# Kernel tuning notes

Hardware: AMD Instinct MI355X
Metric: run time of the kernel (lower is better)

The kernel has to match this reference:

```python
import jax, jax.numpy as jnp
import numpy as np

B = 16; V = 30522; D = 512; H = 8; DH = 64; FF = 2048
NC = 4; NF = 30; NN = 34; FL = 64; HL = 32; NLAYERS = 2

def _pos_encoding(L, d):
    pos = np.arange(L)[:, None].astype(np.float32)
    i = np.arange(0, d, 2)[None, :].astype(np.float32)
    ang = pos / np.power(10000.0, i / d)
    pe = np.zeros((L, d), dtype=np.float32)
    pe[:, 0::2] = np.sin(ang)
    pe[:, 1::2] = np.cos(ang)
    return jnp.asarray(pe)

def _ln(x, g, b):
    m = x.mean(-1, keepdims=True)
    v = ((x - m) ** 2).mean(-1, keepdims=True)
    return (x - m) / jnp.sqrt(v + 1e-5) * g + b

def _encoder(ids, emb, Wqkv, bqkv, Wo, bo, ln1_g, ln1_b, Wff1, bff1, Wff2, bff2, ln2_g, ln2_b):
    Bx, L = ids.shape
    x = emb[ids] * jnp.sqrt(jnp.float32(D)) + _pos_encoding(L, D)
    for l in range(NLAYERS):  # torch post-norm encoder layer, relu FFN
        qkv = x @ Wqkv[l] + bqkv[l]
        q, k, v = jnp.split(qkv, 3, axis=-1)
        q = q.reshape(Bx, L, H, DH); k = k.reshape(Bx, L, H, DH); v = v.reshape(Bx, L, H, DH)
        att = jax.nn.softmax(jnp.einsum('blhd,bmhd->bhlm', q, k) / jnp.sqrt(jnp.float32(DH)), axis=-1)
        o = jnp.einsum('bhlm,bmhd->blhd', att, v).reshape(Bx, L, D) @ Wo[l] + bo[l]
        x = _ln(x + o, ln1_g[l], ln1_b[l])
        f = jax.nn.relu(x @ Wff1[l] + bff1[l]) @ Wff2[l] + bff2[l]
        x = _ln(x + f, ln2_g[l], ln2_b[l])
    return x

def _masked_mean(emb, mask):
    m = mask[..., None]
    return (emb * m).sum(1) / jnp.clip(m.sum(1), 1e-9, None)

def _solve_edges(W, adj, iters=100, lr=0.05, c=10.0):
    # differentiable proxy for the CvxpyLayer SDP relaxation: projected gradient
    # ascent on symmetric E in [0,1], maximizing sum(W*E) with quadratic penalties
    # for sum(adj*E) <= 6 and trace(E[:4,:4]) == 1 (PSD constraint dropped).
    diag4 = jnp.zeros((NN, NN)).at[jnp.arange(NC), jnp.arange(NC)].set(1.0)
    E0 = jnp.full(W.shape, 0.5)
    def step(E, _):
        s = jnp.sum(adj * E, axis=(1, 2), keepdims=True)
        d = jnp.sum(E * diag4, axis=(1, 2), keepdims=True)
        g = W - 2.0 * c * jax.nn.relu(s - 6.0) * adj - 2.0 * c * (d - 1.0) * diag4
        En = E + lr * g
        En = jnp.clip(0.5 * (En + jnp.swapaxes(En, 1, 2)), 0.0, 1.0)
        return En, None
    E, _ = jax.lax.scan(step, E0, None, length=iters)
    return E

def setup_inputs():
    key = jax.random.key(0)
    ks = jax.random.split(key, 24)
    w = lambda k, shape: (jax.random.normal(k, shape) * 0.02).astype(jnp.float32)
    return {
        'hypothesis_input_ids': jax.random.randint(ks[0], (B, NC, HL), 0, V),
        'hypothesis_attention_mask': jnp.ones((B, NC, HL), jnp.float32),
        'fact_attention_mask': jnp.ones((B, NF, FL), jnp.float32),
        'fact_input_ids': jax.random.randint(ks[1], (B, NF, FL), 0, V),
        'grounding_grounding_overlap': jax.random.uniform(ks[2], (B, NN, NN)),
        'abstract_abstract_overlap': jax.random.uniform(ks[3], (B, NN, NN)),
        'abstract_abstract_similarity': jax.random.uniform(ks[4], (B, NN, NN)),
        'question_grounding_overlap': jax.random.uniform(ks[5], (B, NN, NN)),
        'question_abstract_overlap': jax.random.uniform(ks[6], (B, NN, NN)),
        'question_abstract_similarity': jax.random.uniform(ks[7], (B, NN, NN)),
        'grounding_abstract_overlap': jax.random.uniform(ks[8], (B, NN, NN)),
        'question_question_score': w(ks[9], (B, NN, NN)),
        'labels': jax.random.randint(ks[10], (B,), 0, NC),
        'gold_similarity_scores': jax.random.normal(ks[11], (B, NC, NF)),
        'emb_table': w(ks[12], (V, D)),
        'Wqkv': w(ks[13], (NLAYERS, D, 3 * D)), 'bqkv': jnp.zeros((NLAYERS, 3 * D)),
        'Wo': w(ks[14], (NLAYERS, D, D)), 'bo': jnp.zeros((NLAYERS, D)),
        'ln1_g': jnp.ones((NLAYERS, D)), 'ln1_b': jnp.zeros((NLAYERS, D)),
        'Wff1': w(ks[15], (NLAYERS, D, FF)), 'bff1': jnp.zeros((NLAYERS, FF)),
        'Wff2': w(ks[16], (NLAYERS, FF, D)), 'bff2': jnp.zeros((NLAYERS, D)),
        'ln2_g': jnp.ones((NLAYERS, D)), 'ln2_b': jnp.zeros((NLAYERS, D)),
        'score_W': w(ks[17], (4 * D,)), 'score_b': jnp.zeros(()),
        'abs_score_W': w(ks[18], (4 * D,)), 'abs_score_b': jnp.zeros(()),
        'p_aa_overlap': jnp.ones(()), 'p_aa_sim': jnp.ones(()),
        'p_qa_overlap': jnp.ones(()), 'p_qa_sim': jnp.ones(()),
    }

def reference(hypothesis_input_ids, hypothesis_attention_mask, fact_attention_mask, fact_input_ids,
              grounding_grounding_overlap, abstract_abstract_overlap, abstract_abstract_similarity,
              question_grounding_overlap, question_abstract_overlap, question_abstract_similarity,
              grounding_abstract_overlap, question_question_score, labels, gold_similarity_scores,
              emb_table, Wqkv, bqkv, Wo, bo, ln1_g, ln1_b, Wff1, bff1, Wff2, bff2, ln2_g, ln2_b,
              score_W, score_b, abs_score_W, abs_score_b, p_aa_overlap, p_aa_sim, p_qa_overlap, p_qa_sim):
    enc = lambda ids: _encoder(ids, emb_table, Wqkv, bqkv, Wo, bo, ln1_g, ln1_b,
                               Wff1, bff1, Wff2, bff2, ln2_g, ln2_b)
    fseq = _masked_mean(enc(fact_input_ids.reshape(-1, FL)),
                        fact_attention_mask.reshape(-1, FL)).reshape(-1, NF, D)
    hseq = _masked_mean(enc(hypothesis_input_ids.reshape(-1, HL)),
                        hypothesis_attention_mask.reshape(-1, HL)).reshape(-1, NC, D)
    # abstract-abstract pairwise: concat(f_j, f_i, |f_j-f_i|, f_j*f_i) @ abs_score_W, done chunk-wise
    A1, A2, A3, A4 = jnp.split(abs_score_W, 4)
    aa = (fseq @ A1)[:, None, :] + (fseq @ A2)[:, :, None] \
       + jnp.einsum('bijd,d->bij', jnp.abs(fseq[:, None, :, :] - fseq[:, :, None, :]), A3) \
       + jnp.einsum('bid,bjd->bij', fseq * A4, fseq) + abs_score_b
    aa_sm = jax.nn.softmax(aa.reshape(-1, NF * NF), axis=1).reshape(-1, NF, NF)
    aa_sm = aa_sm * (1.0 - jnp.eye(NF))  # zero diagonal
    aa_sim = abstract_abstract_similarity.at[:, NC:, NC:].set(aa_sm)
    # question-abstract pairwise: concat(f_k, h_c, |f_k-h_c|, f_k*h_c) @ score_W
    S1, S2, S3, S4 = jnp.split(score_W, 4)
    qa = (fseq @ S1)[:, None, :] + (hseq @ S2)[:, :, None] \
       + jnp.einsum('bckd,d->bck', jnp.abs(fseq[:, None, :, :] - hseq[:, :, None, :]), S3) \
       + jnp.einsum('bkd,bcd->bck', fseq * S4, hseq) + score_b
    similarity_scores = jax.nn.softmax(qa, axis=2)  # [B, NC, NF]
    qa_sim = jnp.zeros_like(grounding_abstract_overlap)
    qa_sim = qa_sim.at[:, NC:, :NC].set(jnp.transpose(similarity_scores, (0, 2, 1)))
    qa_sim = qa_sim.at[:, :NC, NC:].set(similarity_scores)
    edge_weights = (-p_aa_overlap * abstract_abstract_overlap + p_aa_sim * aa_sim
                    + p_qa_overlap * question_abstract_overlap + p_qa_sim * qa_sim
                    + question_question_score)
    adj = (edge_weights != 0).astype(jnp.float32)
    edges = _solve_edges(edge_weights, adj)
    final_pred = jnp.diagonal(edges[:, :NC, :NC], axis1=1, axis2=2)  # [B, NC]
    gold = jax.nn.softmax(gold_similarity_scores, axis=2)
    logp = jax.nn.log_softmax(final_pred, axis=1)
    ce = -jnp.mean(logp[jnp.arange(final_pred.shape[0]), labels])
    mse = jnp.mean((similarity_scores - gold) ** 2)
    return ce + mse, final_pred
```

## Files before the change

kernel.cpp:

```cpp
#include <hip/hip_runtime.h>
#include <cstdint>
#include <cstddef>


using u16 = unsigned short;

typedef __bf16 bf16x8 __attribute__((ext_vector_type(8)));
typedef float  floatx4 __attribute__((ext_vector_type(4)));

#if defined(__has_builtin)
#if __has_builtin(__builtin_amdgcn_global_load_lds)
#define USE_GLL 1
#endif
#endif

__device__ __forceinline__ float bf2f(u16 u) {
  return __uint_as_float(((unsigned)u) << 16);
}
__device__ __forceinline__ u16 f2bf(float f) {
  unsigned u = __float_as_uint(f);
  u += 0x7FFFu + ((u >> 16) & 1u);
  return (u16)(u >> 16);
}
__device__ __forceinline__ float ldf(const void* p, size_t i, int isb) {
  return isb ? bf2f(((const u16*)p)[i]) : ((const float*)p)[i];
}

__device__ __forceinline__ float waveSum(float v) {
#pragma unroll
  for (int o = 32; o > 0; o >>= 1) v += __shfl_xor(v, o, 64);
  return v;
}
__device__ __forceinline__ float waveMax(float v) {
#pragma unroll
  for (int o = 32; o > 0; o >>= 1) v = fmaxf(v, __shfl_xor(v, o, 64));
  return v;
}
__device__ __forceinline__ float blockSum(float v, float* sh4) {
  v = waveSum(v);
  if ((threadIdx.x & 63) == 0) sh4[threadIdx.x >> 6] = v;
  __syncthreads();
  float r = sh4[0] + sh4[1] + sh4[2] + sh4[3];
  __syncthreads();
  return r;
}
__device__ __forceinline__ float blockMax(float v, float* sh4) {
  v = waveMax(v);
  if ((threadIdx.x & 63) == 0) sh4[threadIdx.x >> 6] = v;
  __syncthreads();
  float r = fmaxf(fmaxf(sh4[0], sh4[1]), fmaxf(sh4[2], sh4[3]));
  __syncthreads();
  return r;
}

__global__ void detect_kernel(const void* __restrict__ ln1g, int* __restrict__ flag) {
  unsigned u = *(const unsigned*)ln1g;
  *flag = (u == 0x3F800000u) ? 0 : 1;
}

__global__ __launch_bounds__(256) void pe_kernel(float* __restrict__ petab) {
  const int pos = blockIdx.x;
  const float LOG1E4_OVER_D = 9.210340371976184f / 512.0f;
  for (int d = threadIdx.x; d < 512; d += 256) {
    int i2 = d & ~1;
    float ang = (float)pos * expf(-(float)i2 * LOG1E4_OVER_D);
    petab[pos * 512 + d] = (d & 1) ? cosf(ang) : sinf(ang);
  }
}

__global__ __launch_bounds__(256) void transpose_kernel(const void* __restrict__ src,
                                                        u16* __restrict__ dst,
                                                        int K, int N,
                                                        size_t srcz, size_t dstz,
                                                        const int* __restrict__ F) {
  const int isb = *F;
  __shared__ u16 tile[32][33];
  size_t eoff = (size_t)blockIdx.z * srcz;
  u16* d = dst + (size_t)blockIdx.z * dstz;
  int bx = blockIdx.x, by = blockIdx.y;
  int tx = threadIdx.x & 31, ty = threadIdx.x >> 5;
  for (int i = ty; i < 32; i += 8)
    tile[i][tx] = f2bf(ldf(src, eoff + (size_t)(by * 32 + i) * N + bx * 32 + tx, isb));
  __syncthreads();
  for (int i = ty; i < 32; i += 8)
    d[(size_t)(bx * 32 + i) * K + by * 32 + tx] = tile[tx][i];
}

__global__ __launch_bounds__(256) void embed_kernel(const int* __restrict__ ids,
                                                    const void* __restrict__ emb,
                                                    u16* __restrict__ x, int L,
                                                    const float* __restrict__ petab,
                                                    const int* __restrict__ F) {
  const int isb = *F;
  int tok = blockIdx.x;
  int pos = tok % L;
  int id = ids[tok];
  for (int d = threadIdx.x; d < 512; d += 256) {
    float e = ldf(emb, (size_t)id * 512 + d, isb) * 22.62741699796952f;
    x[(size_t)tok * 512 + d] = f2bf(e + petab[pos * 512 + d]);
  }
}

__global__ __launch_bounds__(256) void embed2_kernel(const int* __restrict__ fids,
                                                     const int* __restrict__ hids,
                                                     const void* __restrict__ emb,
                                                     u16* __restrict__ x,
                                                     const float* __restrict__ petab,
                                                     const int* __restrict__ F) {
  const int isb = *F;
  int tok = blockIdx.x;
  int id, pos;
  if (tok < 30720) { id = fids[tok]; pos = tok & 63; }
  else             { int t2 = tok - 30720; id = hids[t2]; pos = t2 & 31; }
  for (int d = threadIdx.x; d < 512; d += 256) {
    float e = ldf(emb, (size_t)id * 512 + d, isb) * 22.62741699796952f;
    x[(size_t)tok * 512 + d] = f2bf(e + petab[pos * 512 + d]);
  }
}

template <int RELU>
__global__ __launch_bounds__(256, 2) void gemm_bt(const u16* __restrict__ A,
                                                  const u16* __restrict__ Bt,
                                                  const void* __restrict__ bias,
                                                  u16* __restrict__ C,
                                                  int M, int N, int K, size_t boff,
                                                  const int* __restrict__ F) {
  const int isb = *F;
  __shared__ __align__(16) u16 As[128 * 64];
  __shared__ __align__(16) u16 Bs[128 * 64];
  const int tid = threadIdx.x;
  const int lane = tid & 63;
  const int wave = tid >> 6;
  const int wm = wave >> 1, wn = wave & 1;
  const int l15 = lane & 15, quad = lane >> 4;

  const int nwg = gridDim.x * gridDim.y;
  const int hw  = blockIdx.y * gridDim.x + blockIdx.x;
  int lg;
  if ((nwg & 7) == 0) {
    lg = (hw & 7) * (nwg >> 3) + (hw >> 3);
  } else {
    int q = nwg >> 3, r = nwg & 7;
    int xcd = hw & 7, j = hw >> 3;
    lg = (xcd < r ? xcd * (q + 1) : r * (q + 1) + (xcd - r) * q) + j;
  }
  const int bm = lg / gridDim.x;
  const int bn = lg - bm * gridDim.x;

  floatx4 acc[4][4];
#pragma unroll
  for (int i = 0; i < 4; i++)
#pragma unroll
    for (int j = 0; j < 4; j++) acc[i][j] = (floatx4){0.f, 0.f, 0.f, 0.f};

  const u16* Abase = A + (size_t)bm * 128 * K;
  const u16* Bbase = Bt + (size_t)bn * 128 * K;

  for (int kt = 0; kt < K; kt += 64) {
#pragma unroll
    for (int i = 0; i < 4; i++) {
      int c = i * 256 + tid;
      int row = c >> 3, p = c & 7;
      int col = (((p - row) & 7)) * 8;
      const u16* ga = &Abase[(size_t)row * K + kt + col];
      const u16* gb = &Bbase[(size_t)row * K + kt + col];
#ifdef USE_GLL
      __builtin_amdgcn_global_load_lds(
          (const __attribute__((address_space(1))) void*)ga,
          (__attribute__((address_space(3))) void*)&As[c * 8], 16, 0, 0);
      __builtin_amdgcn_global_load_lds(
          (const __attribute__((address_space(1))) void*)gb,
          (__attribute__((address_space(3))) void*)&Bs[c * 8], 16, 0, 0);
#else
      *(uint4*)&As[c * 8] = *(const uint4*)ga;
      *(uint4*)&Bs[c * 8] = *(const uint4*)gb;
#endif
    }
    __syncthreads();
#pragma unroll
    for (int ks = 0; ks < 2; ks++) {
      bf16x8 af[4], bfr[4];
#pragma unroll
      for (int mi = 0; mi < 4; mi++) {
        int ra = wm * 64 + mi * 16 + l15;
        int q = ks * 4 + quad;
        af[mi] = *(const bf16x8*)&As[ra * 64 + ((q + ra) & 7) * 8];
      }
#pragma unroll
      for (int ni = 0; ni < 4; ni++) {
        int rb = wn * 64 + ni * 16 + l15;
        int q = ks * 4 + quad;
        bfr[ni] = *(const bf16x8*)&Bs[rb * 64 + ((q + rb) & 7) * 8];
      }
#pragma unroll
      for (int mi = 0; mi < 4; mi++)
#pragma unroll
        for (int ni = 0; ni < 4; ni++)
          acc[mi][ni] = __builtin_amdgcn_mfma_f32_16x16x32_bf16(af[mi], bfr[ni], acc[mi][ni], 0, 0, 0);
    }
    __syncthreads();
  }

  float bv[4];
  const int gcb = bn * 128 + wn * 64 + l15;
#pragma unroll
  for (int ni = 0; ni < 4; ni++) bv[ni] = ldf(bias, boff + gcb + ni * 16, isb);
#pragma unroll
  for (int mi = 0; mi < 4; mi++) {
#pragma unroll
    for (int r = 0; r < 4; r++) {
      int grow = bm * 128 + wm * 64 + mi * 16 + quad * 4 + r;
      size_t rb = (size_t)grow * N + gcb;
#pragma unroll
      for (int ni = 0; ni < 4; ni++) {
        float v = acc[mi][ni][r] + bv[ni];
        if (RELU) v = fmaxf(v, 0.f);
        C[rb + ni * 16] = f2bf(v);
      }
    }
  }
}

__global__ __launch_bounds__(256) void attn_kernel(const u16* __restrict__ qkv,
                                                   u16* __restrict__ o, int L,
                                                   int nblk1,
                                                   const u16* __restrict__ qkv2,
                                                   u16* __restrict__ o2, int L2) {
  int bid = blockIdx.x;
  if (bid >= nblk1) { qkv = qkv2; o = o2; L = L2; bid -= nblk1; }
  const int h = bid & 7;
  const int s = bid >> 3;
  __shared__ __align__(16) u16 Qs[64 * 72];
  __shared__ __align__(16) u16 Ks[64 * 72];
  __shared__ __align__(16) u16 Vt[64 * 72];
  __shared__ float Ss[64 * 66];
  const int tid = threadIdx.x;
  const int lane = tid & 63;
  const int wave = tid >> 6;
  const int wm = wave >> 1, wn = wave & 1;
  const int l15 = lane & 15, quad = lane >> 4;
  const int base = s * L;

  for (int idx = tid; idx < 512; idx += 256) {
    int t = idx >> 3, d8 = (idx & 7) * 8;
    if (t < L) {
      size_t g = (size_t)(base + t) * 1536 + h * 64 + d8;
      *(uint4*)&Qs[t * 72 + d8] = *(const uint4*)&qkv[g];
      *(uint4*)&Ks[t * 72 + d8] = *(const uint4*)&qkv[g + 512];
      u16 vv[8];
      *(uint4*)vv = *(const uint4*)&qkv[g + 1024];
#pragma unroll
      for (int i = 0; i < 8; i++) Vt[(d8 + i) * 72 + t] = vv[i];
    } else {
      uint4 z = {0u, 0u, 0u, 0u};
      *(uint4*)&Qs[t * 72 + d8] = z;
      *(uint4*)&Ks[t * 72 + d8] = z;
#pragma unroll
      for (int i = 0; i < 8; i++) Vt[(d8 + i) * 72 + t] = 0;
    }
  }
  __syncthreads();

  {
    floatx4 acc[2][2];
#pragma unroll
    for (int mi = 0; mi < 2; mi++)
#pragma unroll
      for (int ni = 0; ni < 2; ni++) acc[mi][ni] = (floatx4){0.f, 0.f, 0.f, 0.f};
#pragma unroll
    for (int ks = 0; ks < 2; ks++) {
      bf16x8 af[2], bfr[2];
#pragma unroll
      for (int mi = 0; mi < 2; mi++)
        af[mi] = *(const bf16x8*)&Qs[(wm * 32 + mi * 16 + l15) * 72 + ks * 32 + quad * 8];
#pragma unroll
      for (int ni = 0; ni < 2; ni++)
        bfr[ni] = *(const bf16x8*)&Ks[(wn * 32 + ni * 16 + l15) * 72 + ks * 32 + quad * 8];
#pragma unroll
      for (int mi = 0; mi < 2; mi++)
#pragma unroll
        for (int ni = 0; ni < 2; ni++)
          acc[mi][ni] = __builtin_amdgcn_mfma_f32_16x16x32_bf16(af[mi], bfr[ni], acc[mi][ni], 0, 0, 0);
    }
#pragma unroll
    for (int mi = 0; mi < 2; mi++)
#pragma unroll
      for (int ni = 0; ni < 2; ni++)
#pragma unroll
        for (int r = 0; r < 4; r++)
          Ss[(wm * 32 + mi * 16 + quad * 4 + r) * 66 + wn * 32 + ni * 16 + l15] =
              acc[mi][ni][r] * 0.125f;
  }
  __syncthreads();

  {
    int r = tid >> 2, sub = tid & 3;
    int j0 = sub * 16;
    float mx = -3.4e38f;
    if (r < L)
      for (int j = j0; j < j0 + 16; j++)
        if (j < L) mx = fmaxf(mx, Ss[r * 66 + j]);
    mx = fmaxf(mx, __shfl_xor(mx, 1, 64));
    mx = fmaxf(mx, __shfl_xor(mx, 2, 64));
    float sum = 0.f;
    if (r < L)
      for (int j = j0; j < j0 + 16; j++)
        if (j < L) { float e = expf(Ss[r * 66 + j] - mx); Ss[r * 66 + j] = e; sum += e; }
    sum += __shfl_xor(sum, 1, 64);
    sum += __shfl_xor(sum, 2, 64);
    float inv = 1.f / sum;
    if (r < L)
      for (int j = j0; j < j0 + 16; j++)
        Qs[r * 72 + j] = (j < L) ? f2bf(Ss[r * 66 + j] * inv) : (u16)0;
  }
  __syncthreads();

  {
    floatx4 acc[2][2];
#pragma unroll
    for (int mi = 0; mi < 2; mi++)
#pragma unroll
      for (int ni = 0; ni < 2; ni++) acc[mi][ni] = (floatx4){0.f, 0.f, 0.f, 0.f};
#pragma unroll
    for (int ks = 0; ks < 2; ks++) {
      bf16x8 af[2], bfr[2];
#pragma unroll
      for (int mi = 0; mi < 2; mi++)
        af[mi] = *(const bf16x8*)&Qs[(wm * 32 + mi * 16 + l15) * 72 + ks * 32 + quad * 8];
#pragma unroll
      for (int ni = 0; ni < 2; ni++)
        bfr[ni] = *(const bf16x8*)&Vt[(wn * 32 + ni * 16 + l15) * 72 + ks * 32 + quad * 8];
#pragma unroll
      for (int mi = 0; mi < 2; mi++)
#pragma unroll
        for (int ni = 0; ni < 2; ni++)
          acc[mi][ni] = __builtin_amdgcn_mfma_f32_16x16x32_bf16(af[mi], bfr[ni], acc[mi][ni], 0, 0, 0);
    }
#pragma unroll
    for (int mi = 0; mi < 2; mi++) {
#pragma unroll
      for (int r = 0; r < 4; r++) {
        int t = wm * 32 + mi * 16 + quad * 4 + r;
        if (t < L) {
#pragma unroll
          for (int ni = 0; ni < 2; ni++) {
            int d = wn * 32 + ni * 16 + l15;
            o[(size_t)(base + t) * 512 + h * 64 + d] = f2bf(acc[mi][ni][r]);
          }
        }
      }
    }
  }
}

__global__ __launch_bounds__(256) void add_ln_kernel(u16* __restrict__ x,
                                                     const u16* __restrict__ y,
                                                     const void* __restrict__ g,
                                                     const void* __restrict__ b,
                                                     size_t eoff,
                                                     const int* __restrict__ F) {
  const int isb = *F;
  const int row = blockIdx.x, tid = threadIdx.x;
  __shared__ float sh[4];
  size_t o0 = (size_t)row * 512 + tid * 2;
  unsigned xv = *(const unsigned*)&x[o0];
  unsigned yv = *(const unsigned*)&y[o0];
  float v0 = bf2f((u16)xv) + bf2f((u16)yv);
  float v1 = bf2f((u16)(xv >> 16)) + bf2f((u16)(yv >> 16));
  float mean = blockSum(v0 + v1, sh) * (1.f / 512.f);
  float d0 = v0 - mean, d1 = v1 - mean;
  float var = blockSum(d0 * d0 + d1 * d1, sh) * (1.f / 512.f);
  float rstd = rsqrtf(var + 1e-5f);
  float g0 = ldf(g, eoff + tid * 2, isb),     g1 = ldf(g, eoff + tid * 2 + 1, isb);
  float b0 = ldf(b, eoff + tid * 2, isb),     b1 = ldf(b, eoff + tid * 2 + 1, isb);
  unsigned r0 = f2bf(d0 * rstd * g0 + b0);
  unsigned r1 = f2bf(d1 * rstd * g1 + b1);
  *(unsigned*)&x[o0] = r0 | (r1 << 16);
}

__global__ __launch_bounds__(256) void pool_kernel(const u16* __restrict__ x,
                                                   const void* __restrict__ mask,
                                                   float* __restrict__ pooled, int L,
                                                   size_t moff,
                                                   const int* __restrict__ F) {
  const int isb = *F;
  const int s = blockIdx.x;
  float msum = 0.f;
  for (int t = 0; t < L; t++) msum += ldf(mask, moff + s * L + t, isb);
  float inv = 1.f / fmaxf(msum, 1e-9f);
  for (int d = threadIdx.x; d < 512; d += 256) {
    float acc = 0.f;
    for (int t = 0; t < L; t++)
      acc += bf2f(x[(size_t)(s * L + t) * 512 + d]) * ldf(mask, moff + s * L + t, isb);
    pooled[(size_t)s * 512 + d] = acc * inv;
  }
}

__global__ __launch_bounds__(256) void pool2_kernel(const u16* __restrict__ xf,
                                                    const void* __restrict__ fmask,
                                                    float* __restrict__ fpool,
                                                    const u16* __restrict__ xh,
                                                    const void* __restrict__ hmask,
                                                    float* __restrict__ hpool,
                                                    const int* __restrict__ F) {
  const int isb = *F;
  const u16* x; const void* mask; float* pooled; int L, s;
  if (blockIdx.x < 480) { x = xf; mask = fmask; pooled = fpool; L = 64; s = blockIdx.x; }
  else                  { x = xh; mask = hmask; pooled = hpool; L = 32; s = blockIdx.x - 480; }
  float msum = 0.f;
  for (int t = 0; t < L; t++) msum += ldf(mask, (size_t)s * L + t, isb);
  float inv = 1.f / fmaxf(msum, 1e-9f);
  for (int d = threadIdx.x; d < 512; d += 256) {
    float acc = 0.f;
    for (int t = 0; t < L; t++)
      acc += bf2f(x[(size_t)(s * L + t) * 512 + d]) * ldf(mask, (size_t)s * L + t, isb);
    pooled[(size_t)s * 512 + d] = acc * inv;
  }
}

__global__ __launch_bounds__(64) void pair_score_kernel(const float* __restrict__ X,
                                                        const float* __restrict__ Y,
                                                        const void* __restrict__ Wv,
                                                        const void* __restrict__ bscal,
                                                        float* __restrict__ outp,
                                                        int NI, int NJ,
                                                        const int* __restrict__ F) {
  const int isb = *F;
  int gid = blockIdx.x;
  int j = gid % NJ;
  int t = gid / NJ;
  int i = t % NI;
  int b = t / NI;
  const float* xv = X + ((size_t)b * NI + i) * 512;
  const float* yv = Y + ((size_t)b * NJ + j) * 512;
  int l = threadIdx.x;
  float p = 0.f;
  for (int d = l; d < 512; d += 64) {
    float xi = xv[d], yj = yv[d];
    p += ldf(Wv, d, isb) * yj + ldf(Wv, 512 + d, isb) * xi +
         ldf(Wv, 1024 + d, isb) * fabsf(yj - xi) + ldf(Wv, 1536 + d, isb) * xi * yj;
  }
  p = waveSum(p);
  if (l == 0) outp[gid] = p + ldf(bscal, 0, isb);
}

__global__ __launch_bounds__(256) void aa_softmax_kernel(const float* __restrict__ aa,
                                                         float* __restrict__ aasm) {
  const int b = blockIdx.x;
  const float* src = aa + (size_t)b * 900;
  float* dst = aasm + (size_t)b * 900;
  __shared__ float sh[4];
  int tid = threadIdx.x;
  float mx = -3.4e38f;
  for (int i = tid; i < 900; i += 256) mx = fmaxf(mx, src[i]);
  mx = blockMax(mx, sh);
  float sum = 0.f;
  for (int i = tid; i < 900; i += 256) sum += expf(src[i] - mx);
  sum = blockSum(sum, sh);
  float inv = 1.f / sum;
  for (int i = tid; i < 900; i += 256) {
    int r = i / 30, c = i - r * 30;
    dst[i] = (r == c) ? 0.f : expf(src[i] - mx) * inv;
  }
}

__global__ __launch_bounds__(64) void qa_softmax_kernel(const float* __restrict__ qa,
                                                        float* __restrict__ sim) {
  int g = blockIdx.x;
  int l = threadIdx.x;
  float v = (l < 30) ? qa[(size_t)g * 30 + l] : -3.4e38f;
  float mx = waveMax(v);
  float e = (l < 30) ? expf(v - mx) : 0.f;
  float s = waveSum(e);
  if (l < 30) sim[(size_t)g * 30 + l] = e / s;
}

__global__ __launch_bounds__(256) void edgew_kernel(const void* __restrict__ aaov,
                                                    const void* __restrict__ aasim_in,
                                                    const void* __restrict__ qaov,
                                                    const void* __restrict__ qq,
                                                    const float* __restrict__ aasm,
                                                    const float* __restrict__ sim,
                                                    const void* __restrict__ p1,
                                                    const void* __restrict__ p2,
                                                    const void* __restrict__ p3,
                                                    const void* __restrict__ p4,
                                                    float* __restrict__ Wout,
                                                    const int* __restrict__ F) {
  const int isb = *F;
  int e = blockIdx.x * 256 + threadIdx.x;
  if (e >= 16 * 1156) return;
  int b = e / 1156;
  int rem = e - b * 1156;
  int r = rem / 34, c = rem - r * 34;
  float aas;
  if (r >= 4 && c >= 4) aas = aasm[(size_t)b * 900 + (r - 4) * 30 + (c - 4)];
  else                  aas = ldf(aasim_in, e, isb);
  float qas = 0.f;
  if (r >= 4 && c < 4)      qas = sim[((size_t)b * 4 + c) * 30 + (r - 4)];
  else if (r < 4 && c >= 4) qas = sim[((size_t)b * 4 + r) * 30 + (c - 4)];
  float w = -ldf(p1, 0, isb) * ldf(aaov, e, isb) + ldf(p2, 0, isb) * aas +
            ldf(p3, 0, isb) * ldf(qaov, e, isb) + ldf(p4, 0, isb) * qas +
            ldf(qq, e, isb);
  Wout[e] = w;
}

__global__ __launch_bounds__(64) void solve_kernel(const float* __restrict__ Wmat,
                                                   float* __restrict__ pred,
                                                   float* __restrict__ outp) {
  const int b = blockIdx.x;
  const int lane = threadIdx.x;
  float E[19], Ws[19], As[19];
  bool dg[19];
#pragma unroll
  for (int k = 0; k < 19; k++) {
    int e = lane + (k << 6);
    if (e < 1156) {
      int r = e / 34, c = e - r * 34;
      float w1 = Wmat[(size_t)b * 1156 + e];
      float w2 = Wmat[(size_t)b * 1156 + c * 34 + r];
      Ws[k] = 0.5f * (w1 + w2);
      As[k] = 0.5f * (((w1 != 0.f) ? 1.f : 0.f) + ((w2 != 0.f) ? 1.f : 0.f));
      dg[k] = (r == c && r < 4);
      E[k] = 0.5f;
    } else {
      Ws[k] = 0.f; As[k] = 0.f; dg[k] = false; E[k] = 0.f;
    }
  }
  for (int it = 0; it < 100; it++) {
    float ps = 0.f;
#pragma unroll
    for (int k = 0; k < 19; k++) ps += As[k] * E[k];
    float s = waveSum(ps);
    float dd = __shfl(E[0], 0, 64) + __shfl(E[0], 35, 64) +
               __shfl(E[1], 6, 64) + __shfl(E[1], 41, 64);
    float coef_s = (s > 6.f) ? 20.f * (s - 6.f) : 0.f;
    float coef_d = 20.f * (dd - 1.f);
#pragma unroll
    for (int k = 0; k < 19; k++) {
      float g = Ws[k] - coef_s * As[k] - (dg[k] ? coef_d : 0.f);
      E[k] = fminf(fmaxf(E[k] + 0.05f * g, 0.f), 1.f);
    }
  }
  float v0 = E[0], v1 = E[1];
  if (lane == 0)  { pred[b * 4 + 0] = v0; outp[1 + b * 4 + 0] = v0; }
  if (lane == 35) { pred[b * 4 + 1] = v0; outp[1 + b * 4 + 1] = v0; }
  if (lane == 6)  { pred[b * 4 + 2] = v1; outp[1 + b * 4 + 2] = v1; }
  if (lane == 41) { pred[b * 4 + 3] = v1; outp[1 + b * 4 + 3] = v1; }
}

__global__ __launch_bounds__(256) void loss_kernel(const float* __restrict__ sim,
                                                   const void* __restrict__ gold,
                                                   const float* __restrict__ pred,
                                                   const int* __restrict__ labels,
                                                   float* __restrict__ outp,
                                                   const int* __restrict__ F) {
  const int isb = *F;
  __shared__ float sh[4];
  const int tid = threadIdx.x;
  float local = 0.f;
  if (tid < 64) {
    float mx = -3.4e38f;
    for (int k = 0; k < 30; k++) mx = fmaxf(mx, ldf(gold, (size_t)tid * 30 + k, isb));
    float sum = 0.f;
    for (int k = 0; k < 30; k++) sum += expf(ldf(gold, (size_t)tid * 30 + k, isb) - mx);
    float inv = 1.f / sum;
    for (int k = 0; k < 30; k++) {
      float gsm = expf(ldf(gold, (size_t)tid * 30 + k, isb) - mx) * inv;
      float d = sim[(size_t)tid * 30 + k] - gsm;
      local += d * d;
    }
  }
  float mse = blockSum(local, sh) * (1.f / 1920.f);
  float cel = 0.f;
  if (tid < 16) {
    const float* f = pred + tid * 4;
    int lb = labels[tid] & 3;
    float mx = fmaxf(fmaxf(f[0], f[1]), fmaxf(f[2], f[3]));
    float lse = logf(expf(f[0] - mx) + expf(f[1] - mx) + expf(f[2] - mx) + expf(f[3] - mx));
    float lp = f[lb] - mx - lse;
    cel = -lp * (1.f / 16.f);
  }
  float ce = blockSum(cel, sh);
  if (tid == 0) outp[0] = ce + mse;
}

extern "C" void kernel_launch(void* const* d_in, const int* in_sizes, int n_in,
                              void* d_out, int out_size, void* d_ws, size_t ws_size,
                              hipStream_t stream) {
  (void)in_sizes; (void)n_in; (void)out_size;
  const int*  hyp_ids   = (const int*)d_in[0];
  const void* hyp_mask  = d_in[1];
  const void* fact_mask = d_in[2];
  const int*  fact_ids  = (const int*)d_in[3];
  const void* aa_ov     = d_in[5];
  const void* aa_sim_in = d_in[6];
  const void* qa_ov     = d_in[8];
  const void* qq        = d_in[11];
  const int*  labels    = (const int*)d_in[12];
  const void* gold      = d_in[13];
  const void* emb       = d_in[14];
  const void* Wqkv      = d_in[15];
  const void* bqkv      = d_in[16];
  const void* Wo        = d_in[17];
  const void* bo        = d_in[18];
  const void* ln1g      = d_in[19];
  const void* ln1b      = d_in[20];
  const void* Wff1      = d_in[21];
  const void* bff1      = d_in[22];
  const void* Wff2      = d_in[23];
  const void* bff2      = d_in[24];
  const void* ln2g      = d_in[25];
  const void* ln2b      = d_in[26];
  const void* scoreW    = d_in[27];
  const void* scoreB    = d_in[28];
  const void* absW      = d_in[29];
  const void* absB      = d_in[30];
  const void* p_aaov    = d_in[31];
  const void* p_aasim   = d_in[32];
  const void* p_qaov    = d_in[33];
  const void* p_qasim   = d_in[34];
  float* out = (float*)d_out;

  char* ws = (char*)d_ws;
  size_t off = 0;
  auto alloc = [&](size_t bytes) -> void* {
    void* p = ws + off;
    off += (bytes + 255) & ~(size_t)255;
    return p;
  };

  float* PRED = (float*)alloc(64ull * 4);
  int*   FLAG = (int*)alloc(256);
  float* SIM  = (float*)alloc(16ull * 120 * 4);
  float* QA   = (float*)alloc(16ull * 120 * 4);
  float* AASM = (float*)alloc(16ull * 900 * 4);
  float* AA   = (float*)alloc(16ull * 900 * 4);
  float* WMAT = (float*)alloc(16ull * 1156 * 4);
  float* FSEQ = (float*)alloc(480ull * 512 * 4);
  float* HSEQ = (float*)alloc(64ull * 512 * 4);
  float* PETAB= (float*)alloc(64ull * 512 * 4);
  u16* WT_QKV = (u16*)alloc(2ull * 1536 * 512 * 2);
  u16* WT_O   = (u16*)alloc(2ull * 512 * 512 * 2);
  u16* WT_F1  = (u16*)alloc(2ull * 2048 * 512 * 2);
  u16* WT_F2  = (u16*)alloc(2ull * 512 * 2048 * 2);

  const int opts_tok[6] = {32768, 30720, 15360, 10240, 6144, 3072};
  const int opts_nch[6] = {1, 1, 2, 3, 5, 10};
  int CH_TOK = 3072, NCH = 10;
  for (int i = 0; i < 6; i++) {
    size_t need = off + (size_t)opts_tok[i] * 7168 + 4096;
    if (need <= ws_size) { CH_TOK = opts_tok[i]; NCH = opts_nch[i]; break; }
  }
  u16* X   = (u16*)alloc((size_t)CH_TOK * 512 * 2);
  u16* BIG = (u16*)alloc((size_t)CH_TOK * 2048 * 2);
  u16* ATT = (u16*)alloc((size_t)CH_TOK * 512 * 2);
  u16* Y   = (u16*)alloc((size_t)CH_TOK * 512 * 2);

  detect_kernel<<<1, 1, 0, stream>>>(ln1g, FLAG);
  pe_kernel<<<64, 256, 0, stream>>>(PETAB);

  transpose_kernel<<<dim3(48, 16, 2), 256, 0, stream>>>(
      Wqkv, WT_QKV, 512, 1536, 512ull * 1536, 1536ull * 512, FLAG);
  transpose_kernel<<<dim3(16, 16, 2), 256, 0, stream>>>(
      Wo, WT_O, 512, 512, 512ull * 512, 512ull * 512, FLAG);
  transpose_kernel<<<dim3(64, 16, 2), 256, 0, stream>>>(
      Wff1, WT_F1, 512, 2048, 512ull * 2048, 2048ull * 512, FLAG);
  transpose_kernel<<<dim3(16, 64, 2), 256, 0, stream>>>(
      Wff2, WT_F2, 2048, 512, 2048ull * 512, 512ull * 2048, FLAG);

  if (CH_TOK >= 32768) {
    const int M = 32768;
    const size_t HOFF = 30720;
    embed2_kernel<<<M, 256, 0, stream>>>(fact_ids, hyp_ids, emb, X, PETAB, FLAG);
    for (int l = 0; l < 2; l++) {
      gemm_bt<0><<<dim3(12, M / 128), 256, 0, stream>>>(
          X, WT_QKV + (size_t)l * 1536 * 512, bqkv, BIG, M, 1536, 512,
          (size_t)l * 1536, FLAG);
      attn_kernel<<<480 * 8 + 64 * 8, 256, 0, stream>>>(
          BIG, ATT, 64, 480 * 8, BIG + HOFF * 1536, ATT + HOFF * 512, 32);
      gemm_bt<0><<<dim3(4, M / 128), 256, 0, stream>>>(
          ATT, WT_O + (size_t)l * 512 * 512, bo, Y, M, 512, 512,
          (size_t)l * 512, FLAG);
      add_ln_kernel<<<M, 256, 0, stream>>>(X, Y, ln1g, ln1b, (size_t)l * 512, FLAG);
      gemm_bt<1><<<dim3(16, M / 128), 256, 0, stream>>>(
          X, WT_F1 + (size_t)l * 2048 * 512, bff1, BIG, M, 2048, 512,
          (size_t)l * 2048, FLAG);
      gemm_bt<0><<<dim3(4, M / 128), 256, 0, stream>>>(
          BIG, WT_F2 + (size_t)l * 512 * 2048, bff2, Y, M, 512, 2048,
          (size_t)l * 512, FLAG);
      add_ln_kernel<<<M, 256, 0, stream>>>(X, Y, ln2g, ln2b, (size_t)l * 512, FLAG);
    }
    pool2_kernel<<<544, 256, 0, stream>>>(X, fact_mask, FSEQ,
                                          X + HOFF * 512, hyp_mask, HSEQ, FLAG);
  } else {
    auto encode = [&](const int* ids, int nseq, int L, const void* mask,
                      size_t moff, float* pooled) {
      int M = nseq * L;
      embed_kernel<<<M, 256, 0, stream>>>(ids, emb, X, L, PETAB, FLAG);
      for (int l = 0; l < 2; l++) {
        gemm_bt<0><<<dim3(12, M / 128), 256, 0, stream>>>(
            X, WT_QKV + (size_t)l * 1536 * 512, bqkv, BIG, M, 1536, 512,
            (size_t)l * 1536, FLAG);
        attn_kernel<<<nseq * 8, 256, 0, stream>>>(BIG, ATT, L, nseq * 8, BIG, ATT, L);
        gemm_bt<0><<<dim3(4, M / 128), 256, 0, stream>>>(
            ATT, WT_O + (size_t)l * 512 * 512, bo, Y, M, 512, 512,
            (size_t)l * 512, FLAG);
        add_ln_kernel<<<M, 256, 0, stream>>>(X, Y, ln1g, ln1b, (size_t)l * 512, FLAG);
        gemm_bt<1><<<dim3(16, M / 128), 256, 0, stream>>>(
            X, WT_F1 + (size_t)l * 2048 * 512, bff1, BIG, M, 2048, 512,
            (size_t)l * 2048, FLAG);
        gemm_bt<0><<<dim3(4, M / 128), 256, 0, stream>>>(
            BIG, WT_F2 + (size_t)l * 512 * 2048, bff2, Y, M, 512, 2048,
            (size_t)l * 512, FLAG);
        add_ln_kernel<<<M, 256, 0, stream>>>(X, Y, ln2g, ln2b, (size_t)l * 512, FLAG);
      }
      pool_kernel<<<nseq, 256, 0, stream>>>(X, mask, pooled, L, moff, FLAG);
    };
    const int seq_per = 480 / NCH;
    for (int c = 0; c < NCH; c++) {
      encode(fact_ids + (size_t)c * seq_per * 64, seq_per, 64, fact_mask,
             (size_t)c * seq_per * 64, FSEQ + (size_t)c * seq_per * 512);
    }
    encode(hyp_ids, 64, 32, hyp_mask, 0, HSEQ);
  }

  pair_score_kernel<<<16 * 30 * 30, 64, 0, stream>>>(FSEQ, FSEQ, absW, absB, AA, 30, 30, FLAG);
  pair_score_kernel<<<16 * 4 * 30, 64, 0, stream>>>(HSEQ, FSEQ, scoreW, scoreB, QA, 4, 30, FLAG);
  aa_softmax_kernel<<<16, 256, 0, stream>>>(AA, AASM);
  qa_softmax_kernel<<<64, 64, 0, stream>>>(QA, SIM);

  edgew_kernel<<<(16 * 1156 + 255) / 256, 256, 0, stream>>>(
      aa_ov, aa_sim_in, qa_ov, qq, AASM, SIM, p_aaov, p_aasim, p_qaov, p_qasim,
      WMAT, FLAG);
  solve_kernel<<<16, 64, 0, stream>>>(WMAT, PRED, out);
  loss_kernel<<<1, 256, 0, stream>>>(SIM, gold, PRED, labels, out, FLAG);
}
```

Measured before the change: 990.2 us.

## Swizzle V-transpose LDS layout and merge pair-score and softmax launches

Result: no change. 990.1 us (-0.0%).

```diff
diff --git a/kernel.cpp b/kernel.cpp
--- a/kernel.cpp
+++ b/kernel.cpp
@@ -243,6 +243,7 @@
 
   for (int idx = tid; idx < 512; idx += 256) {
     int t = idx >> 3, d8 = (idx & 7) * 8;
+    int rot = ((t >> 3) + (idx & 7)) & 7;
     if (t < L) {
       size_t g = (size_t)(base + t) * 1536 + h * 64 + d8;
       *(uint4*)&Qs[t * 72 + d8] = *(const uint4*)&qkv[g];
@@ -250,13 +251,13 @@
       u16 vv[8];
       *(uint4*)vv = *(const uint4*)&qkv[g + 1024];
 #pragma unroll
-      for (int i = 0; i < 8; i++) Vt[(d8 + i) * 72 + t] = vv[i];
+      for (int i = 0; i < 8; i++) Vt[(d8 + i) * 72 + rot * 8 + (t & 7)] = vv[i];
     } else {
       uint4 z = {0u, 0u, 0u, 0u};
       *(uint4*)&Qs[t * 72 + d8] = z;
       *(uint4*)&Ks[t * 72 + d8] = z;
 #pragma unroll
-      for (int i = 0; i < 8; i++) Vt[(d8 + i) * 72 + t] = 0;
+      for (int i = 0; i < 8; i++) Vt[(d8 + i) * 72 + rot * 8 + (t & 7)] = 0;
     }
   }
   __syncthreads();
@@ -328,8 +329,11 @@
       for (int mi = 0; mi < 2; mi++)
         af[mi] = *(const bf16x8*)&Qs[(wm * 32 + mi * 16 + l15) * 72 + ks * 32 + quad * 8];
 #pragma unroll
-      for (int ni = 0; ni < 2; ni++)
-        bfr[ni] = *(const bf16x8*)&Vt[(wn * 32 + ni * 16 + l15) * 72 + ks * 32 + quad * 8];
+      for (int ni = 0; ni < 2; ni++) {
+        int rb = wn * 32 + ni * 16 + l15;
+        int p = ((ks * 4 + quad) + (rb >> 3)) & 7;
+        bfr[ni] = *(const bf16x8*)&Vt[rb * 72 + p * 8];
+      }
 #pragma unroll
       for (int mi = 0; mi < 2; mi++)
 #pragma unroll
@@ -418,15 +422,20 @@
   }
 }
 
-__global__ __launch_bounds__(64) void pair_score_kernel(const float* __restrict__ X,
-                                                        const float* __restrict__ Y,
-                                                        const void* __restrict__ Wv,
-                                                        const void* __restrict__ bscal,
-                                                        float* __restrict__ outp,
-                                                        int NI, int NJ,
-                                                        const int* __restrict__ F) {
+__global__ __launch_bounds__(64) void pair2_kernel(const float* __restrict__ FS,
+                                                   const float* __restrict__ HS,
+                                                   const void* __restrict__ absW,
+                                                   const void* __restrict__ absB,
+                                                   const void* __restrict__ scW,
+                                                   const void* __restrict__ scB,
+                                                   float* __restrict__ AA,
+                                                   float* __restrict__ QA,
+                                                   const int* __restrict__ F) {
   const int isb = *F;
   int gid = blockIdx.x;
+  const float *X, *Y; const void *Wv, *bs; float* outp; int NI, NJ;
+  if (gid < 14400) { X = FS; Y = FS; Wv = absW; bs = absB; outp = AA; NI = 30; NJ = 30; }
+  else { gid -= 14400; X = HS; Y = FS; Wv = scW; bs = scB; outp = QA; NI = 4; NJ = 30; }
   int j = gid % NJ;
   int t = gid / NJ;
   int i = t % NI;
@@ -441,38 +450,39 @@
          ldf(Wv, 1024 + d, isb) * fabsf(yj - xi) + ldf(Wv, 1536 + d, isb) * xi * yj;
   }
   p = waveSum(p);
-  if (l == 0) outp[gid] = p + ldf(bscal, 0, isb);
-}
-
-__global__ __launch_bounds__(256) void aa_softmax_kernel(const float* __restrict__ aa,
-                                                         float* __restrict__ aasm) {
-  const int b = blockIdx.x;
-  const float* src = aa + (size_t)b * 900;
-  float* dst = aasm + (size_t)b * 900;
+  if (l == 0) outp[gid] = p + ldf(bs, 0, isb);
+}
+
+__global__ __launch_bounds__(256) void sm2_kernel(const float* __restrict__ aa,
+                                                  float* __restrict__ aasm,
+                                                  const float* __restrict__ qa,
+                                                  float* __restrict__ sim) {
   __shared__ float sh[4];
-  int tid = threadIdx.x;
-  float mx = -3.4e38f;
-  for (int i = tid; i < 900; i += 256) mx = fmaxf(mx, src[i]);
-  mx = blockMax(mx, sh);
-  float sum = 0.f;
-  for (int i = tid; i < 900; i += 256) sum += expf(src[i] - mx);
-  sum = blockSum(sum, sh);
-  float inv = 1.f / sum;
-  for (int i = tid; i < 900; i += 256) {
-    int r = i / 30, c = i - r * 30;
-    dst[i] = (r == c) ? 0.f : expf(src[i] - mx) * inv;
-  }
-}
-
-__global__ __launch_bounds__(64) void qa_softmax_kernel(const float* __restrict__ qa,
-                                                        float* __restrict__ sim) {
-  int g = blockIdx.x;
-  int l = threadIdx.x;
-  float v = (l < 30) ? qa[(size_t)g * 30 + l] : -3.4e38f;
-  float mx = waveMax(v);
-  float e = (l < 30) ? expf(v - mx) : 0.f;
-  float s = waveSum(e);
-  if (l < 30) sim[(size_t)g * 30 + l] = e / s;
+  if (blockIdx.x < 16) {
+    const int b = blockIdx.x;
+    const float* src = aa + (size_t)b * 900;
+    float* dst = aasm + (size_t)b * 900;
+    int tid = threadIdx.x;
+    float mx = -3.4e38f;
+    for (int i = tid; i < 900; i += 256) mx = fmaxf(mx, src[i]);
+    mx = blockMax(mx, sh);
+    float sum = 0.f;
+    for (int i = tid; i < 900; i += 256) sum += expf(src[i] - mx);
+    sum = blockSum(sum, sh);
+    float inv = 1.f / sum;
+    for (int i = tid; i < 900; i += 256) {
+      int r = i / 30, c = i - r * 30;
+      dst[i] = (r == c) ? 0.f : expf(src[i] - mx) * inv;
+    }
+  } else {
+    int g = (blockIdx.x - 16) * 4 + (threadIdx.x >> 6);
+    int l = threadIdx.x & 63;
+    float v = (l < 30) ? qa[(size_t)g * 30 + l] : -3.4e38f;
+    float mx = waveMax(v);
+    float e = (l < 30) ? expf(v - mx) : 0.f;
+    float s = waveSum(e);
+    if (l < 30) sim[(size_t)g * 30 + l] = e / s;
+  }
 }
 
 __global__ __launch_bounds__(256) void edgew_kernel(const void* __restrict__ aaov,
@@ -725,10 +735,9 @@
     encode(hyp_ids, 64, 32, hyp_mask, 0, HSEQ);
   }
 
-  pair_score_kernel<<<16 * 30 * 30, 64, 0, stream>>>(FSEQ, FSEQ, absW, absB, AA, 30, 30, FLAG);
-  pair_score_kernel<<<16 * 4 * 30, 64, 0, stream>>>(HSEQ, FSEQ, scoreW, scoreB, QA, 4, 30, FLAG);
-  aa_softmax_kernel<<<16, 256, 0, stream>>>(AA, AASM);
-  qa_softmax_kernel<<<64, 64, 0, stream>>>(QA, SIM);
+  pair2_kernel<<<16 * 30 * 30 + 16 * 4 * 30, 64, 0, stream>>>(
+      FSEQ, HSEQ, absW, absB, scoreW, scoreB, AA, QA, FLAG);
+  sm2_kernel<<<32, 256, 0, stream>>>(AA, AASM, QA, SIM);
 
   edgew_kernel<<<(16 * 1156 + 255) / 256, 256, 0, stream>>>(
       aa_ov, aa_sim_in, qa_ov, qq, AASM, SIM, p_aaov, p_aasim, p_qaov, p_qasim,
```
